# Performance work log

Measured on AMD Instinct MI355X. Metric: run time of the kernel, lower is better.

Reference implementation:

```python
import jax, jax.numpy as jnp
from jax import lax
import numpy as np


def conv2d(x, w, b=None, padding=0, dilation=1, groups=1):
    out = lax.conv_general_dilated(
        x, w, window_strides=(1, 1),
        padding=[(padding, padding), (padding, padding)],
        rhs_dilation=(dilation, dilation),
        dimension_numbers=('NCHW', 'OIHW', 'NCHW'),
        feature_group_count=groups)
    return out if b is None else out + b[None, :, None, None]


def hardswish(x):
    return x * jnp.clip(x + 3.0, 0.0, 6.0) / 6.0


def leaky(x, s):
    return jnp.where(x >= 0, x, s * x)


def bn_eval(x, g, b, eps=1e-5):
    # BatchNorm2d eval mode with running_mean=0, running_var=1
    scale = g * (1.0 / float(np.sqrt(1.0 + eps)))
    return x * scale[None, :, None, None] + b[None, :, None, None]


def deform_dw_conv(x, offset, w):
    # torchvision DeformConv2d, depthwise (groups=C), k=3, stride=1, pad=1, dil=1
    # x [B,C,H,W], offset [B,18,H,W] (y,x interleaved, kernel row-major), w [C,1,3,3]
    B, C, H, W = x.shape
    xf = x.reshape(B, C, H * W)
    yy = jnp.arange(H, dtype=x.dtype)[:, None]
    xx = jnp.arange(W, dtype=x.dtype)[None, :]
    out = jnp.zeros_like(x)
    for k in range(9):
        ky, kx = k // 3 - 1, k % 3 - 1
        py = yy + ky + offset[:, 2 * k]          # [B,H,W]
        px = xx + kx + offset[:, 2 * k + 1]
        y0 = jnp.floor(py)
        x0 = jnp.floor(px)
        wy = py - y0
        wx = px - x0
        y0i = y0.astype(jnp.int32)
        x0i = x0.astype(jnp.int32)
        val = jnp.zeros_like(x)
        for dy, dx, wgt in ((0, 0, (1 - wy) * (1 - wx)), (0, 1, (1 - wy) * wx),
                            (1, 0, wy * (1 - wx)), (1, 1, wy * wx)):
            iy = y0i + dy
            ix = x0i + dx
            valid = (iy >= 0) & (iy < H) & (ix >= 0) & (ix < W)
            idx = (jnp.clip(iy, 0, H - 1) * W + jnp.clip(ix, 0, W - 1)).reshape(B, 1, H * W)
            g = jnp.take_along_axis(xf, idx, axis=2).reshape(B, C, H, W)
            val = val + g * (wgt * valid.astype(x.dtype))[:, None]
        out = out + val * w[:, 0, ky + 1, kx + 1][None, :, None, None]
    return out


def patch_embed(x, off_dw, off_pw, dcn_w, pw_w):
    g = x.shape[1]
    off = conv2d(x, off_dw, padding=1, groups=g)
    off = jnp.clip(conv2d(off, off_pw), -1.0, 1.0)
    y = deform_dw_conv(x, off, dcn_w)
    return hardswish(conv2d(y, pw_w))


def depth_conv(x, dw_w, dw_b, pw_w, pw_b):
    g = x.shape[1]
    return conv2d(conv2d(x, dw_w, dw_b, padding=1, groups=g), pw_w, pw_b)


def cross_attn(hs, ctx, dw_w, dw_b, pw_w, pw_b):
    q = depth_conv(hs, dw_w[0], dw_b[0], pw_w[0], pw_b[0])
    k = depth_conv(ctx, dw_w[1], dw_b[1], pw_w[1], pw_b[1])
    v = depth_conv(ctx, dw_w[2], dw_b[2], pw_w[2], pw_b[2])
    head = q.shape[1] // 8  # num_heads = 8
    qt = q.transpose(0, 2, 1, 3)  # [B,H,C,W]
    kt = k.transpose(0, 2, 1, 3)
    vt = v.transpose(0, 2, 1, 3)
    scores = jnp.einsum('bhcw,bhdw->bhcd', qt, kt) / float(np.sqrt(head))
    probs = jax.nn.softmax(scores, axis=-1)
    o = jnp.einsum('bhcd,bhdw->bhcw', probs, vt)
    return o.transpose(0, 2, 1, 3)  # back to [B,C,H,W]


def dilated_block(x, ws, bs):
    h = x
    for i, d in enumerate((1, 2, 3, 2, 1)):
        h = conv2d(h, ws[i], bs[i], padding=d, dilation=d)
        if i < 4:
            h = leaky(h, 0.01)
    return h + x


def fft_block(h, fd1_w, fd2_w, fd1_g, fd1_bt, fd2_g, fd2_bt, fconv_w):
    Hh, Ww = h.shape[-2], h.shape[-1]
    xf = jnp.fft.rfft2(h)  # norm='backward'
    re, im = jnp.real(xf), jnp.imag(xf)
    mag = jnp.sqrt(re * re + im * im)
    pha = jnp.arctan2(im, re)

    def branch(m, i):
        t = leaky(bn_eval(conv2d(m, fd1_w[i]), fd1_g[i], fd1_bt[i]), 0.1)
        m1 = jnp.concatenate([m, t], 1)          # C+32
        t2 = leaky(bn_eval(conv2d(m1, fd2_w[i]), fd2_g[i], fd2_bt[i]), 0.1)
        m2 = jnp.concatenate([m1, t2], 1)        # C+64
        return conv2d(m2, fconv_w[i])            # back to C

    mag_o = branch(mag, 0)
    pha_o = branch(pha, 1)
    real = mag_o * jnp.cos(pha_o)
    imag = mag_o * jnp.sin(pha_o)
    out = jnp.fft.irfft2(lax.complex(real, imag), s=(Hh, Ww)) + h
    return out, mag_o, pha_o


def scarm_forward(x, ch_off_dw, ch_off_pw, ch_dcn_w, ch_pw,
                  ct_off_dw, ct_off_pw, ct_dcn_w, ct_pw,
                  db_w, db_b, ca_dw_w, ca_dw_b, ca_pw_w, ca_pw_b,
                  convHH_w, convHH_b, fd1_w, fd2_w, fd1_g, fd1_bt,
                  fd2_g, fd2_bt, fconv_w, conv_w, conv_b):
    b = x.shape[0]
    residual = x
    h = patch_embed(x, ch_off_dw, ch_off_pw, ch_dcn_w, ch_pw)  # [B,64,H,W]
    fft_out, mag, pha = fft_block(h, fd1_w, fd2_w, fd1_g, fd1_bt, fd2_g, fd2_bt, fconv_w)
    t = b // 3
    x_HL, x_LH, x_HH = h[:t], h[t:2 * t], h[2 * t:]
    # note: faithful to source, which aliases fft_LH/fft_HH back to x (h)
    fft_HL, fft_LH, fft_HH = fft_out[:t], h[t:2 * t], h[2 * t:]
    x_HH_LH = cross_attn(x_LH, x_HH, ca_dw_w[0], ca_dw_b[0], ca_pw_w[0], ca_pw_b[0])
    x_HH_HL = cross_attn(x_HL, x_HH, ca_dw_w[1], ca_dw_b[1], ca_pw_w[1], ca_pw_b[1])
    f_HH_LH = cross_attn(fft_LH, fft_HH, ca_dw_w[0], ca_dw_b[0], ca_pw_w[0], ca_pw_b[0])
    f_HH_HL = cross_attn(fft_HL, fft_HH, ca_dw_w[1], ca_dw_b[1], ca_pw_w[1], ca_pw_b[1])
    x_HL2 = dilated_block(x_HL, db_w[1], db_b[1])
    x_LH2 = dilated_block(x_LH, db_w[0], db_b[0])
    x_HH2 = dilated_block(conv2d(jnp.concatenate([x_HH_LH, x_HH_HL], 1), convHH_w, convHH_b, padding=1), db_w[2], db_b[2])
    f_HH2 = dilated_block(conv2d(jnp.concatenate([f_HH_LH, f_HH_HL], 1), convHH_w, convHH_b, padding=1), db_w[2], db_b[2])
    out = patch_embed(jnp.concatenate([x_HL2, x_LH2, x_HH2], 0), ct_off_dw, ct_off_pw, ct_dcn_w, ct_pw)
    fftout = patch_embed(jnp.concatenate([fft_HL, fft_LH, f_HH2], 0), ct_off_dw, ct_off_pw, ct_dcn_w, ct_pw)
    out = conv2d(jnp.concatenate([out, fftout], 1), conv_w, conv_b, padding=1)
    return out + residual, mag, pha


def setup_inputs() -> dict:
    key = jax.random.key(0)
    ks = iter(jax.random.split(key, 32))

    def rn(shape, scale):
        return jax.random.normal(next(ks), shape, jnp.float32) * scale

    return {
        'x': rn([12, 3, 128, 128], 1.0),
        'ch_off_dw': rn([3, 1, 3, 3], 0.3), 'ch_off_pw': rn([18, 3, 1, 1], 0.3),
        'ch_dcn_w': rn([3, 1, 3, 3], 0.3), 'ch_pw': rn([64, 3, 1, 1], 0.3),
        'ct_off_dw': rn([64, 1, 3, 3], 0.1), 'ct_off_pw': rn([18, 64, 1, 1], 0.1),
        'ct_dcn_w': rn([64, 1, 3, 3], 0.1), 'ct_pw': rn([3, 64, 1, 1], 0.05),
        'db_w': rn([3, 5, 64, 64, 3, 3], 0.05), 'db_b': rn([3, 5, 64], 0.01),
        'ca_dw_w': rn([2, 3, 64, 1, 3, 3], 0.3), 'ca_dw_b': rn([2, 3, 64], 0.01),
        'ca_pw_w': rn([2, 3, 64, 64, 1, 1], 0.1), 'ca_pw_b': rn([2, 3, 64], 0.01),
        'convHH_w': rn([64, 128, 3, 3], 0.03), 'convHH_b': rn([64], 0.01),
        'fd1_w': rn([2, 32, 64, 1, 1], 0.1), 'fd2_w': rn([2, 32, 96, 1, 1], 0.1),
        'fd1_g': 1.0 + rn([2, 32], 0.1), 'fd1_bt': rn([2, 32], 0.1),
        'fd2_g': 1.0 + rn([2, 32], 0.1), 'fd2_bt': rn([2, 32], 0.1),
        'fconv_w': rn([2, 64, 128, 1, 1], 0.1),
        'conv_w': rn([3, 6, 3, 3], 0.1), 'conv_b': rn([3], 0.01),
    }


def reference(x, ch_off_dw, ch_off_pw, ch_dcn_w, ch_pw,
              ct_off_dw, ct_off_pw, ct_dcn_w, ct_pw,
              db_w, db_b, ca_dw_w, ca_dw_b, ca_pw_w, ca_pw_b,
              convHH_w, convHH_b, fd1_w, fd2_w, fd1_g, fd1_bt,
              fd2_g, fd2_bt, fconv_w, conv_w, conv_b):
    return scarm_forward(x, ch_off_dw, ch_off_pw, ch_dcn_w, ch_pw,
                         ct_off_dw, ct_off_pw, ct_dcn_w, ct_pw,
                         db_w, db_b, ca_dw_w, ca_dw_b, ca_pw_w, ca_pw_b,
                         convHH_w, convHH_b, fd1_w, fd2_w, fd1_g, fd1_bt,
                         fd2_g, fd2_bt, fconv_w, conv_w, conv_b)
```

## Files before the change

### kernel.cpp

```cpp
#include <hip/hip_runtime.h>

namespace {

constexpr int Hn = 128, Wn = 128, HWn = 16384, HWFn = 8320;
constexpr float TWOPI = 6.2831853071795864769f;
constexpr float BN_SCALE = 0.99999500003749968f;

typedef __attribute__((ext_vector_type(8))) short short8;
typedef __attribute__((ext_vector_type(4))) float float4v;

__device__ __forceinline__ short f2bf(float v){
  unsigned u = __float_as_uint(v);
  u += 0x7FFF + ((u >> 16) & 1);
  return (short)(u >> 16);
}
__device__ __forceinline__ float bf2f(unsigned short u){
  return __uint_as_float(((unsigned)u) << 16);
}

__global__ void k_pack(const float* __restrict__ w, unsigned short* __restrict__ o,
                       int Cin, int csz, int n){
  int idx = blockIdx.x*256 + threadIdx.x;
  if (idx >= n) return;
  int ck = idx / csz;
  int i  = idx - ck*csz;
  const float* wp = w + (size_t)ck*csz;
  int j = i & 7, lane = (i>>3)&63, mt = (i>>9)&3, p = i>>11;
  int blk = p/18, r = p - blk*18, tap = r>>1, ks = r&1;
  int co = mt*16 + (lane & 15);
  int ci = blk*64 + ks*32 + ((lane>>4)<<3) + j;
  o[idx] = (unsigned short)f2bf(wp[((size_t)co*Cin + ci)*9 + tap]);
}

__global__ void k_packpw(const float* __restrict__ w, unsigned short* __restrict__ o,
                         int Cout, int MT, int n){
  int i = blockIdx.x*256 + threadIdx.x;
  if (i >= n) return;
  int per = MT << 10;
  int set = i / per;
  int r = i - set*per;
  int j = r & 7, lane = (r>>3)&63, blk = r>>9;
  int ks = blk / MT, mt = blk - ks*MT;
  int co = mt*16 + (lane & 15);
  int ci = ks*32 + ((lane>>4)<<3) + j;
  float v = (co < Cout) ? w[(size_t)set*Cout*64 + co*64 + ci] : 0.f;
  o[i] = (unsigned short)f2bf(v);
}

__global__ void k_wfdc(const float* __restrict__ fd1w, const float* __restrict__ fd2w,
                       const float* __restrict__ fcw,  const float* __restrict__ fd1g,
                       const float* __restrict__ fd2g, float* __restrict__ o){
  int i = blockIdx.x*256 + threadIdx.x;
  if (i >= 26624) return;
  int br = i / 13312, r = i - br*13312;
  float v;
  if (r < 2048){
    int ci = r >> 5, j = r & 31;
    v = fd1w[br*2048 + j*64 + ci] * (fd1g[br*32 + j]*BN_SCALE);
  } else if (r < 5120){
    int rr = r - 2048; int ci = rr >> 5, j = rr & 31;
    v = fd2w[br*3072 + j*96 + ci] * (fd2g[br*32 + j]*BN_SCALE);
  } else {
    int rr = r - 5120; int ci = rr >> 6, j = rr & 63;
    v = fcw[br*8192 + j*128 + ci];
  }
  o[i] = v;
}

__global__ __launch_bounds__(256) void k_fdc(
    const float* __restrict__ in, const float* __restrict__ wT,
    const float* __restrict__ bt1, const float* __restrict__ bt2,
    float* __restrict__ outp){
  __shared__ float tls[32*256];
  __shared__ float uls[32*256];
  int b = blockIdx.x, tile = blockIdx.y;
  int tid = threadIdx.x;
  int p = tile*256 + tid;
  bool act = p < HWFn;
  if (!act) p = HWFn - 1;
  const float* ip = in + (size_t)b*64*HWFn + p;
  float t[32];
  #pragma unroll
  for (int j=0;j<32;j++) t[j] = bt1[j];
  for (int ci=0; ci<64; ci++){
    float v = ip[(size_t)ci*HWFn];
    const float* w = wT + ci*32;
    #pragma unroll
    for (int j=0;j<32;j++) t[j] = fmaf(v, w[j], t[j]);
  }
  #pragma unroll
  for (int j=0;j<32;j++){
    float a = t[j]; tls[j*256+tid] = (a>=0.f)? a : 0.1f*a;
  }
  float u[32];
  #pragma unroll
  for (int j=0;j<32;j++) u[j] = bt2[j];
  for (int ci=0; ci<64; ci++){
    float v = ip[(size_t)ci*HWFn];
    const float* w = wT + 2048 + ci*32;
    #pragma unroll
    for (int j=0;j<32;j++) u[j] = fmaf(v, w[j], u[j]);
  }
  for (int ci=0; ci<32; ci++){
    float v = tls[ci*256+tid];
    const float* w = wT + 2048 + (64+ci)*32;
    #pragma unroll
    for (int j=0;j<32;j++) u[j] = fmaf(v, w[j], u[j]);
  }
  #pragma unroll
  for (int j=0;j<32;j++){
    float a = u[j]; uls[j*256+tid] = (a>=0.f)? a : 0.1f*a;
  }
  float acc[64];
  #pragma unroll
  for (int j=0;j<64;j++) acc[j] = 0.f;
  for (int ci=0; ci<64; ci++){
    float v = ip[(size_t)ci*HWFn];
    const float* w = wT + 5120 + ci*64;
    #pragma unroll
    for (int j=0;j<64;j++) acc[j] = fmaf(v, w[j], acc[j]);
  }
  for (int ci=0; ci<32; ci++){
    float v = tls[ci*256+tid];
    const float* w = wT + 5120 + (64+ci)*64;
    #pragma unroll
    for (int j=0;j<64;j++) acc[j] = fmaf(v, w[j], acc[j]);
  }
  for (int ci=0; ci<32; ci++){
    float v = uls[ci*256+tid];
    const float* w = wT + 5120 + (96+ci)*64;
    #pragma unroll
    for (int j=0;j<64;j++) acc[j] = fmaf(v, w[j], acc[j]);
  }
  if (act){
    float* op = outp + (size_t)b*64*HWFn + p;
    #pragma unroll
    for (int j=0;j<64;j++) op[(size_t)j*HWFn] = acc[j];
  }
}

constexpr int XST = 72;
__global__ __launch_bounds__(256) void k_mconv(
    const float* __restrict__ in, const float* __restrict__ in2,
    const unsigned short* __restrict__ wpk, const float* __restrict__ bias,
    const float* __restrict__ res, float* __restrict__ out,
    int nblk, int dl, int leaky){
  __shared__ short lds[3*134*XST];
  int b = blockIdx.x >> 7, y = blockIdx.x & 127;
  int tid = threadIdx.x;
  int wv = tid >> 6, lane = tid & 63;
  int nq = lane >> 4, nr = lane & 15;
  float4v acc[4][2];
  #pragma unroll
  for (int mt=0; mt<4; mt++)
    #pragma unroll
    for (int nt=0; nt<2; nt++) acc[mt][nt] = (float4v){0.f,0.f,0.f,0.f};

  for (int blk=0; blk<nblk; blk++){
    const float* src = blk ? in2 : in;
    __syncthreads();
    for (int e = tid; e < 3*64*32; e += 256){
      int dy = e >> 11;
      int r  = e & 2047;
      int ci = r >> 5;
      int xx = (r & 31) << 2;
      int yy = y + (dy-1)*dl;
      float4 v = make_float4(0.f,0.f,0.f,0.f);
      if (yy >= 0 && yy < Hn)
        v = *(const float4*)&src[(((size_t)b*64 + ci)*Hn + yy)*Wn + xx];
      short* d = &lds[(dy*134 + xx + 3)*XST + ci];
      d[0]     = f2bf(v.x);
      d[XST]   = f2bf(v.y);
      d[2*XST] = f2bf(v.z);
      d[3*XST] = f2bf(v.w);
    }
    for (int e = tid; e < 3*64*6; e += 256){
      int dy = e / 384; int r = e - dy*384;
      int ci = r / 6;   int k = r - ci*6;
      int x = (k < 3) ? k : 128 + k;
      lds[(dy*134 + x)*XST + ci] = 0;
    }
    __syncthreads();
    const unsigned short* wb = wpk + (size_t)blk*36864;
    for (int tap=0; tap<9; tap++){
      int dy = tap/3, dx = tap - (tap/3)*3;
      #pragma unroll
      for (int ks=0; ks<2; ks++){
        short8 a[4];
        #pragma unroll
        for (int mt=0; mt<4; mt++)
          a[mt] = *(const short8*)(wb + (((size_t)(tap*2+ks)*4+mt)<<9) + ((size_t)lane<<3));
        #pragma unroll
        for (int nt=0; nt<2; nt++){
          int x = wv*32 + nt*16 + nr + (dx-1)*dl + 3;
          short8 bf = *(const short8*)&lds[(dy*134 + x)*XST + ks*32 + nq*8];
          #pragma unroll
          for (int mt=0; mt<4; mt++)
            acc[mt][nt] = __builtin_amdgcn_mfma_f32_16x16x32_bf16(a[mt], bf, acc[mt][nt], 0, 0, 0);
        }
      }
    }
  }
  #pragma unroll
  for (int mt=0; mt<4; mt++)
  #pragma unroll
  for (int nt=0; nt<2; nt++){
    int x = wv*32 + nt*16 + nr;
    #pragma unroll
    for (int r2=0; r2<4; r2++){
      int co = mt*16 + nq*4 + r2;
      float a = acc[mt][nt][r2] + (bias ? bias[co] : 0.f);
      if (leaky) a = (a >= 0.f) ? a : 0.01f*a;
      size_t idx = (((size_t)b*64 + co)*Hn + y)*Wn + x;
      if (res) a += res[idx];
      out[idx] = a;
    }
  }
}

template<int MT>
__global__ __launch_bounds__(256) void k_dwpw(
    const float* __restrict__ in, const float* __restrict__ dww, const float* __restrict__ dwb,
    const unsigned short* __restrict__ pwpk, const float* __restrict__ pwb,
    float* __restrict__ out, int Cout, size_t outb, int post){
  __shared__ short tb[128*72];
  __shared__ float wsm[640];
  int b = blockIdx.x >> 7, y = blockIdx.x & 127;
  int tid = threadIdx.x;
  for (int i = tid; i < 640; i += 256)
    wsm[i] = (i < 576) ? dww[i] : (dwb ? dwb[i-576] : 0.f);
  __syncthreads();
  for (int e = tid; e < 2048; e += 256){
    int ci = e >> 5;
    int xx = (e & 31) << 2;
    const float* ip = in + ((size_t)b*64 + ci)*HWn;
    const float* wp = wsm + ci*9;
    float4 a0 = make_float4(0.f,0.f,0.f,0.f), a1 = a0, a2 = a0;
    float L0=0.f,L1=0.f,L2=0.f,R0=0.f,R1=0.f,R2=0.f;
    if (y > 0){
      const float* r = ip + (y-1)*Wn;
      a0 = *(const float4*)(r + xx);
      if (xx) L0 = r[xx-1];
      if (xx < 124) R0 = r[xx+4];
    }
    {
      const float* r = ip + y*Wn;
      a1 = *(const float4*)(r + xx);
      if (xx) L1 = r[xx-1];
      if (xx < 124) R1 = r[xx+4];
    }
    if (y < Hn-1){
      const float* r = ip + (y+1)*Wn;
      a2 = *(const float4*)(r + xx);
      if (xx) L2 = r[xx-1];
      if (xx < 124) R2 = r[xx+4];
    }
    float bb = wsm[576+ci];
    float o0=bb,o1=bb,o2=bb,o3=bb;
    float w0=wp[0],w1=wp[1],w2=wp[2];
    o0 = fmaf(w0,L0,  fmaf(w1,a0.x, fmaf(w2,a0.y, o0)));
    o1 = fmaf(w0,a0.x,fmaf(w1,a0.y, fmaf(w2,a0.z, o1)));
    o2 = fmaf(w0,a0.y,fmaf(w1,a0.z, fmaf(w2,a0.w, o2)));
    o3 = fmaf(w0,a0.z,fmaf(w1,a0.w, fmaf(w2,R0,   o3)));
    w0=wp[3];w1=wp[4];w2=wp[5];
    o0 = fmaf(w0,L1,  fmaf(w1,a1.x, fmaf(w2,a1.y, o0)));
    o1 = fmaf(w0,a1.x,fmaf(w1,a1.y, fmaf(w2,a1.z, o1)));
    o2 = fmaf(w0,a1.y,fmaf(w1,a1.z, fmaf(w2,a1.w, o2)));
    o3 = fmaf(w0,a1.z,fmaf(w1,a1.w, fmaf(w2,R1,   o3)));
    w0=wp[6];w1=wp[7];w2=wp[8];
    o0 = fmaf(w0,L2,  fmaf(w1,a2.x, fmaf(w2,a2.y, o0)));
    o1 = fmaf(w0,a2.x,fmaf(w1,a2.y, fmaf(w2,a2.z, o1)));
    o2 = fmaf(w0,a2.y,fmaf(w1,a2.z, fmaf(w2,a2.w, o2)));
    o3 = fmaf(w0,a2.z,fmaf(w1,a2.w, fmaf(w2,R2,   o3)));
    short* d = &tb[xx*72 + ci];
    d[0]   = f2bf(o0);
    d[72]  = f2bf(o1);
    d[144] = f2bf(o2);
    d[216] = f2bf(o3);
  }
  __syncthreads();
  int wv = tid>>6, lane = tid&63, nq = lane>>4, nr = lane&15;
  float4v acc[MT][2];
  #pragma unroll
  for (int mt=0; mt<MT; mt++)
    #pragma unroll
    for (int nt=0; nt<2; nt++) acc[mt][nt] = (float4v){0.f,0.f,0.f,0.f};
  #pragma unroll
  for (int ks=0; ks<2; ks++){
    short8 a[MT];
    #pragma unroll
    for (int mt=0; mt<MT; mt++)
      a[mt] = *(const short8*)(pwpk + ((ks*MT+mt)<<9) + (lane<<3));
    #pragma unroll
    for (int nt=0; nt<2; nt++){
      int x = wv*32 + nt*16 + nr;
      short8 bf = *(const short8*)&tb[x*72 + ks*32 + nq*8];
      #pragma unroll
      for (int mt=0; mt<MT; mt++)
        acc[mt][nt] = __builtin_amdgcn_mfma_f32_16x16x32_bf16(a[mt], bf, acc[mt][nt], 0, 0, 0);
    }
  }
  #pragma unroll
  for (int mt=0; mt<MT; mt++)
  #pragma unroll
  for (int nt=0; nt<2; nt++){
    int x = wv*32 + nt*16 + nr;
    #pragma unroll
    for (int r2=0; r2<4; r2++){
      int co = mt*16 + nq*4 + r2;
      if (co < Cout){
        float a = acc[mt][nt][r2] + (pwb ? pwb[co] : 0.f);
        if (post == 1) a = fminf(fmaxf(a, -1.f), 1.f);
        else if (post == 2) a = a*fminf(fmaxf(a+3.f, 0.f), 6.f)*(1.f/6.f);
        out[(size_t)b*outb + (size_t)co*HWn + y*Wn + x] = a;
      }
    }
  }
}

__global__ __launch_bounds__(512) void k_defpw(
    const float* __restrict__ xg, const float* __restrict__ off, const float* __restrict__ dcnw,
    const unsigned short* __restrict__ pwpk, float* __restrict__ out,
    int Cout, size_t outb, int post){
  __shared__ unsigned short xs[5*64*130];
  __shared__ short tb[128*72];
  __shared__ float wsm[576];
  int b = blockIdx.x >> 7, y = blockIdx.x & 127;
  int tid = threadIdx.x;
  int px = tid & 127, sub = tid >> 7;
  for (int i = tid; i < 576; i += 512) wsm[i] = dcnw[i];
  for (int e = tid; e < 10240; e += 512){
    int tr = e >> 11;
    int r  = e & 2047;
    int ci = r >> 5;
    int xx = (r & 31) << 2;
    int gy = min(max(y - 2 + tr, 0), Hn-1);
    float4 v = *(const float4*)&xg[(((size_t)b*64 + ci)*Hn + gy)*Wn + xx];
    unsigned short* d = &xs[(tr*64 + ci)*130 + xx];
    d[0] = (unsigned short)f2bf(v.x);
    d[1] = (unsigned short)f2bf(v.y);
    d[2] = (unsigned short)f2bf(v.z);
    d[3] = (unsigned short)f2bf(v.w);
  }
  const float* op = off + (size_t)b*18*HWn + y*Wn + px;
  int t0[9], t1[9], c0[9], c1[9];
  float w00[9], w01[9], w10[9], w11[9];
  #pragma unroll
  for (int k=0; k<9; k++){
    int ky = k/3 - 1, kx = k - (k/3)*3 - 1;
    float oy = op[(size_t)(2*k)*HWn];
    float ox = op[(size_t)(2*k+1)*HWn];
    float py = (float)(y + ky) + oy;
    float pxx = (float)(px + kx) + ox;
    float fy = floorf(py), fx = floorf(pxx);
    float wy = py - fy, wx = pxx - fx;
    int y0 = (int)fy, x0 = (int)fx;
    float vy0 = (y0 >= 0 && y0 < Hn) ? 1.f : 0.f;
    float vy1 = (y0+1 >= 0 && y0+1 < Hn) ? 1.f : 0.f;
    float vx0 = (x0 >= 0 && x0 < Wn) ? 1.f : 0.f;
    float vx1 = (x0+1 >= 0 && x0+1 < Wn) ? 1.f : 0.f;
    w00[k] = (1.f-wy)*(1.f-wx)*vy0*vx0;
    w01[k] = (1.f-wy)*wx*vy0*vx1;
    w10[k] = wy*(1.f-wx)*vy1*vx0;
    w11[k] = wy*wx*vy1*vx1;
    t0[k] = min(max(min(max(y0,   0), Hn-1) - (y-2), 0), 4);
    t1[k] = min(max(min(max(y0+1, 0), Hn-1) - (y-2), 0), 4);
    c0[k] = min(max(x0,   0), Wn-1);
    c1[k] = min(max(x0+1, 0), Wn-1);
  }
  __syncthreads();
  for (int ci = sub; ci < 64; ci += 4){
    float acc = 0.f;
    #pragma unroll
    for (int k=0; k<9; k++){
      const unsigned short* b0 = &xs[(t0[k]*64 + ci)*130];
      const unsigned short* b1 = &xs[(t1[k]*64 + ci)*130];
      float v = w00[k]*bf2f(b0[c0[k]]) + w01[k]*bf2f(b0[c1[k]])
              + w10[k]*bf2f(b1[c0[k]]) + w11[k]*bf2f(b1[c1[k]]);
      acc = fmaf(v, wsm[ci*9 + k], acc);
    }
    tb[px*72 + ci] = f2bf(acc);
  }
  __syncthreads();
  int wv = tid>>6, lane = tid&63, nq = lane>>4, nr = lane&15;
  float4v acc = (float4v){0.f,0.f,0.f,0.f};
  int x = wv*16 + nr;
  #pragma unroll
  for (int ks=0; ks<2; ks++){
    short8 a = *(const short8*)(pwpk + (ks<<9) + (lane<<3));
    short8 bf = *(const short8*)&tb[x*72 + ks*32 + nq*8];
    acc = __builtin_amdgcn_mfma_f32_16x16x32_bf16(a, bf, acc, 0, 0, 0);
  }
  #pragma unroll
  for (int r2=0; r2<4; r2++){
    int co = nq*4 + r2;
    if (co < Cout){
      float a = acc[r2];
      if (post == 2) a = a*fminf(fmaxf(a+3.f, 0.f), 6.f)*(1.f/6.f);
      out[(size_t)b*outb + (size_t)co*HWn + y*Wn + x] = a;
    }
  }
}

__global__ void k_dw3x3(const float* __restrict__ in, const float* __restrict__ w,
                        const float* __restrict__ bias, float* __restrict__ out, int C){
  int bc = blockIdx.x; int y = blockIdx.y; int x = threadIdx.x;
  int c = bc % C;
  const float* ip = in + (size_t)bc*HWn;
  const float* wp = w + c*9;
  float acc = bias ? bias[c] : 0.f;
  #pragma unroll
  for (int ky=0; ky<3; ky++){
    int yy = y + ky - 1; if (yy < 0 || yy >= Hn) continue;
    #pragma unroll
    for (int kx=0; kx<3; kx++){
      int xx = x + kx - 1; if (xx < 0 || xx >= Wn) continue;
      acc = fmaf(ip[yy*Wn+xx], wp[ky*3+kx], acc);
    }
  }
  out[(size_t)bc*HWn + y*Wn + x] = acc;
}

template<int CT>
__global__ void k_pwt(const float* __restrict__ in, const float* __restrict__ wg,
                      const float* __restrict__ bias, const float* __restrict__ bng,
                      const float* __restrict__ bnb, float* __restrict__ out,
                      int Cin, int Cout, int npix, int inb, int outb, int post, float slope){
  extern __shared__ float wsm[];
  int nt = (Cout + CT - 1)/CT;
  int b = blockIdx.x / nt, t = blockIdx.x - b*nt;
  int co0 = t*CT;
  for (int i = threadIdx.x; i < CT*Cin; i += 256){
    int co = i / Cin;
    wsm[i] = (co0 + co < Cout) ? wg[(size_t)(co0+co)*Cin + (i - co*Cin)] : 0.f;
  }
  __syncthreads();
  int p = blockIdx.y*256 + threadIdx.x;
  if (p >= npix) return;
  const float* ip = in + (size_t)b*inb + p;
  float acc[CT];
  #pragma unroll
  for (int j=0; j<CT; j++) acc[j] = 0.f;
  for (int ci=0; ci<Cin; ci++){
    float v = ip[(size_t)ci*npix];
    #pragma unroll
    for (int j=0; j<CT; j++) acc[j] = fmaf(v, wsm[j*Cin+ci], acc[j]);
  }
  #pragma unroll
  for (int j=0; j<CT; j++){
    int co = co0 + j;
    if (co < Cout){
      float a = acc[j] + (bias ? bias[co] : 0.f);
      if (bng) a = a*(bng[co]*BN_SCALE) + bnb[co];
      if (post == 1) a = fminf(fmaxf(a, -1.f), 1.f);
      else if (post == 2) a = a*fminf(fmaxf(a+3.f, 0.f), 6.f)*(1.f/6.f);
      else if (post == 3) a = (a >= 0.f) ? a : a*slope;
      out[(size_t)b*outb + (size_t)co*npix + p] = a;
    }
  }
}

__global__ void k_deform(const float* __restrict__ x, const float* __restrict__ off,
                         const float* __restrict__ w, float* __restrict__ out, int C){
  int bc = blockIdx.x; int b = bc / C; int c = bc - b*C;
  int y = blockIdx.y; int x0 = threadIdx.x;
  const float* xp = x + (size_t)bc*HWn;
  const float* op = off + (size_t)b*18*HWn + y*Wn + x0;
  const float* wp = w + c*9;
  float acc = 0.f;
  #pragma unroll
  for (int k=0; k<9; k++){
    int ky = k/3 - 1, kx = k - (k/3)*3 - 1;
    float oy = op[(size_t)(2*k)*HWn];
    float ox = op[(size_t)(2*k+1)*HWn];
    float py = (float)y + (float)ky + oy;
    float px = (float)x0 + (float)kx + ox;
    float fy = floorf(py), fx = floorf(px);
    float wy = py - fy, wx = px - fx;
    int y0 = (int)fy, xx0 = (int)fx;
    float val = 0.f;
    #pragma unroll
    for (int dy=0; dy<2; dy++){
      int iy = y0 + dy; if (iy < 0 || iy >= Hn) continue;
      float wyv = dy ? wy : (1.f - wy);
      #pragma unroll
      for (int dx=0; dx<2; dx++){
        int ix = xx0 + dx; if (ix < 0 || ix >= Wn) continue;
        float wxv = dx ? wx : (1.f - wx);
        val = fmaf(xp[iy*Wn+ix], wyv*wxv, val);
      }
    }
    acc = fmaf(val, wp[k], acc);
  }
  out[(size_t)bc*HWn + y*Wn + x0] = acc;
}

__global__ void k_conv3x3s(const float* __restrict__ in, const float* __restrict__ wgt,
                           const float* __restrict__ bias, const float* __restrict__ res,
                           float* __restrict__ out, int Cin, int Cout){
  int g = blockIdx.x;
  int b = g / Cout; int o0 = g - b*Cout;
  int y = blockIdx.y, x = threadIdx.x;
  float acc = bias ? bias[o0] : 0.f;
  for (int ci=0; ci<Cin; ci++){
    const float* iip = in + ((size_t)b*Cin + ci)*HWn;
    const float* wp = wgt + ((size_t)o0*Cin + ci)*9;
    #pragma unroll
    for (int ky=0; ky<3; ky++){
      int yy = y + ky - 1; if (yy < 0 || yy >= Hn) continue;
      #pragma unroll
      for (int kx=0; kx<3; kx++){
        int xx = x + kx - 1; if (xx < 0 || xx >= Wn) continue;
        acc = fmaf(iip[yy*Wn+xx], wp[ky*3+kx], acc);
      }
    }
  }
  size_t idx = ((size_t)b*Cout + o0)*HWn + y*Wn + x;
  if (res) acc += res[idx];
  out[idx] = acc;
}

__global__ __launch_bounds__(256) void k_attn(
    const float* __restrict__ q, const float* __restrict__ k,
    const float* __restrict__ v, float* __restrict__ o){
  __shared__ float qs[64][129];
  __shared__ float ks[64][129];
  __shared__ float vs[64][129];
  __shared__ float ps[64][66];
  int bh = blockIdx.x; int b = bh >> 7, h = bh & 127;
  size_t base = ((size_t)b*64*128 + h)*128;
  int tid = threadIdx.x;
  for (int e = tid; e < 8192; e += 256){
    int c = e >> 7, w = e & 127;
    size_t g = base + (size_t)c*HWn + w;
    qs[c][w] = q[g]; ks[c][w] = k[g]; vs[c][w] = v[g];
  }
  __syncthreads();
  {
    int c0 = (tid >> 4) << 2, d0 = (tid & 15) << 2;
    float acc[4][4];
    #pragma unroll
    for (int a=0; a<4; a++)
      #pragma unroll
      for (int bb=0; bb<4; bb++) acc[a][bb] = 0.f;
    for (int i=0; i<128; i++){
      float qv[4], kv[4];
      #pragma unroll
      for (int a=0; a<4; a++){ qv[a] = qs[c0+a][i]; kv[a] = ks[d0+a][i]; }
      #pragma unroll
      for (int a=0; a<4; a++)
        #pragma unroll
        for (int bb=0; bb<4; bb++) acc[a][bb] = fmaf(qv[a], kv[bb], acc[a][bb]);
    }
    #pragma unroll
    for (int a=0; a<4; a++)
      #pragma unroll
      for (int bb=0; bb<4; bb++)
        ps[c0+a][d0+bb] = acc[a][bb] * 0.35355339059327373f;
  }
  __syncthreads();
  {
    int wv = tid >> 6, lane = tid & 63;
    for (int it=0; it<16; it++){
      int row = wv*16 + it;
      float vv = ps[row][lane];
      float m = vv;
      #pragma unroll
      for (int off=32; off; off>>=1) m = fmaxf(m, __shfl_xor(m, off));
      float e = expf(vv - m);
      float s = e;
      #pragma unroll
      for (int off=32; off; off>>=1) s += __shfl_xor(s, off);
      ps[row][lane] = e / s;
    }
  }
  __syncthreads();
  {
    int c0 = (tid >> 4) << 2, w0 = (tid & 15) << 3;
    float acc[4][8];
    #pragma unroll
    for (int a=0; a<4; a++)
      #pragma unroll
      for (int j=0; j<8; j++) acc[a][j] = 0.f;
    for (int d=0; d<64; d++){
      float pv[4], vv[8];
      #pragma unroll
      for (int a=0; a<4; a++) pv[a] = ps[c0+a][d];
      #pragma unroll
      for (int j=0; j<8; j++) vv[j] = vs[d][w0+j];
      #pragma unroll
      for (int a=0; a<4; a++)
        #pragma unroll
        for (int j=0; j<8; j++) acc[a][j] = fmaf(pv[a], vv[j], acc[a][j]);
    }
    #pragma unroll
    for (int a=0; a<4; a++)
      #pragma unroll
      for (int j=0; j<8; j++)
        o[base + (size_t)(c0+a)*HWn + w0 + j] = acc[a][j];
  }
}

__device__ __forceinline__ float2 cmul(float2 a, float2 b){
  return make_float2(a.x*b.x - a.y*b.y, a.x*b.y + a.y*b.x);
}

__device__ __forceinline__ void wfft(float2& z0, float2& z1, const float2* twl, int l){
  {
    float dx = z0.x - z1.x, dy = z0.y - z1.y;
    z0.x += z1.x; z0.y += z1.y;
    z1 = cmul(make_float2(dx, dy), twl[6]);
  }
  #pragma unroll
  for (int s = 5; s >= 0; --s){
    int h = 1 << s;
    bool up = (l & h) != 0;
    float2 w = twl[s];
    {
      float ox = __shfl_xor(z0.x, h), oy = __shfl_xor(z0.y, h);
      float sx = up ? ox - z0.x : z0.x + ox;
      float sy = up ? oy - z0.y : z0.y + oy;
      float2 t = cmul(make_float2(sx, sy), w);
      z0.x = up ? t.x : sx;  z0.y = up ? t.y : sy;
    }
    {
      float ox = __shfl_xor(z1.x, h), oy = __shfl_xor(z1.y, h);
      float sx = up ? ox - z1.x : z1.x + ox;
      float sy = up ? oy - z1.y : z1.y + oy;
      float2 t = cmul(make_float2(sx, sy), w);
      z1.x = up ? t.x : sx;  z1.y = up ? t.y : sy;
    }
  }
}

__device__ __forceinline__ void wreorder(float2 z0, float2 z1, float2& n0, float2& n1, int l){
  int a = (int)(__brev((unsigned)(l >> 1)) >> 26);
  float p0x = __shfl(z0.x, a),   p0y = __shfl(z0.y, a);
  float p1x = __shfl(z1.x, a),   p1y = __shfl(z1.y, a);
  float q0x = __shfl(z0.x, a+1), q0y = __shfl(z0.y, a+1);
  float q1x = __shfl(z1.x, a+1), q1y = __shfl(z1.y, a+1);
  bool odd = (l & 1) != 0;
  n0 = odd ? make_float2(p1x, p1y) : make_float2(p0x, p0y);
  n1 = odd ? make_float2(q1x, q1y) : make_float2(q0x, q0y);
}

__global__ __launch_bounds__(256) void k_fft2(
    const float* __restrict__ x, float* __restrict__ mag, float* __restrict__ pha){
  __shared__ float2 sp[8320];
  int img = blockIdx.x;
  int tid = threadIdx.x;
  int wv = tid >> 6, l = tid & 63;
  float2 twl[7];
  #pragma unroll
  for (int s = 0; s < 7; ++s){
    int jh = (l & ((1 << s) - 1)) << (6 - s);
    float sv, cv; sincosf(-TWOPI * (float)jh * (1.f/128.f), &sv, &cv);
    twl[s] = make_float2(cv, sv);
  }
  const float* xp = x + (size_t)img*HWn;
  for (int f = wv; f < 64; f += 4){
    const float* r0 = xp + (2*f)*Wn;
    const float* r1 = xp + (2*f+1)*Wn;
    float2 z0 = make_float2(r0[l],      r1[l]);
    float2 z1 = make_float2(r0[64 + l], r1[64 + l]);
    wfft(z0, z1, twl, l);
    float2 n0, n1; wreorder(z0, z1, n0, n1, l);
    float zhx = __shfl(n1.x, (64 - l) & 63);
    float zhy = __shfl(n1.y, (64 - l) & 63);
    float2 Zn = (l == 0) ? n0 : make_float2(zhx, zhy);
    float2 A  = make_float2(0.5f*(n0.x + Zn.x), 0.5f*(n0.y - Zn.y));
    float2 Bv = make_float2(0.5f*(n0.y + Zn.y), 0.5f*(Zn.x - n0.x));
    sp[(2*f)*65 + l]   = A;
    sp[(2*f+1)*65 + l] = Bv;
    if (l == 0){
      sp[(2*f)*65 + 64]   = make_float2(n1.x, 0.f);
      sp[(2*f+1)*65 + 64] = make_float2(n1.y, 0.f);
    }
  }
  __syncthreads();
  for (int c = wv; c < 65; c += 4){
    float2 z0 = sp[l*65 + c];
    float2 z1 = sp[(64 + l)*65 + c];
    wfft(z0, z1, twl, l);
    float2 n0, n1; wreorder(z0, z1, n0, n1, l);
    sp[l*65 + c]        = make_float2(sqrtf(n0.x*n0.x + n0.y*n0.y), atan2f(n0.y, n0.x));
    sp[(64 + l)*65 + c] = make_float2(sqrtf(n1.x*n1.x + n1.y*n1.y), atan2f(n1.y, n1.x));
  }
  __syncthreads();
  float* mp = mag + (size_t)img*HWFn;
  float* pp = pha + (size_t)img*HWFn;
  for (int i = tid; i < 8320; i += 256){
    float2 v = sp[i];
    mp[i] = v.x; pp[i] = v.y;
  }
}

__global__ __launch_bounds__(256) void k_ifft2(
    const float* __restrict__ mo, const float* __restrict__ po,
    const float* __restrict__ hsrc, float* __restrict__ outp){
  __shared__ float2 sp[8320];
  int img = blockIdx.x;
  int tid = threadIdx.x;
  int wv = tid >> 6, l = tid & 63;
  float2 twl[7];
  #pragma unroll
  for (int s = 0; s < 7; ++s){
    int jh = (l & ((1 << s) - 1)) << (6 - s);
    float sv, cv; sincosf(TWOPI * (float)jh * (1.f/128.f), &sv, &cv);
    twl[s] = make_float2(cv, sv);
  }
  const float* mp = mo + (size_t)img*HWFn;
  const float* pp = po + (size_t)img*HWFn;
  for (int i = tid; i < 8320; i += 256){
    float m = mp[i], p = pp[i];
    float sv, cv; sincosf(p, &sv, &cv);
    sp[i] = make_float2(m*cv, m*sv);
  }
  __syncthreads();
  for (int c = wv; c < 65; c += 4){
    float2 z0 = sp[l*65 + c];
    float2 z1 = sp[(64 + l)*65 + c];
    wfft(z0, z1, twl, l);
    float2 n0, n1; wreorder(z0, z1, n0, n1, l);
    sp[l*65 + c]        = n0;
    sp[(64 + l)*65 + c] = n1;
  }
  __syncthreads();
  const float scl = 1.f/16384.f;
  for (int f = wv; f < 64; f += 4){
    float2 A  = sp[(2*f)*65 + l];
    float2 Bv = sp[(2*f+1)*65 + l];
    if (l == 0){ A.y = 0.f; Bv.y = 0.f; }
    float2 z0 = make_float2(A.x - Bv.y, A.y + Bv.x);
    int lm = 64 - l;
    float2 Am = sp[(2*f)*65 + lm];
    float2 Bm = sp[(2*f+1)*65 + lm];
    float2 z1 = (l == 0) ? make_float2(Am.x, Bm.x)
                         : make_float2(Am.x + Bm.y, Bm.x - Am.y);
    wfft(z0, z1, twl, l);
    float2 n0, n1; wreorder(z0, z1, n0, n1, l);
    size_t g0 = (size_t)img*HWn + (size_t)(2*f)*Wn + l;
    size_t g1 = g0 + Wn;
    outp[g0]      = n0.x*scl + hsrc[g0];
    outp[g0 + 64] = n1.x*scl + hsrc[g0 + 64];
    outp[g1]      = n0.y*scl + hsrc[g1];
    outp[g1 + 64] = n1.y*scl + hsrc[g1 + 64];
  }
}

}

extern "C" void kernel_launch(void* const* d_in, const int* in_sizes, int n_in,
                              void* d_out, int out_size, void* d_ws, size_t ws_size,
                              hipStream_t stream){
  const float *xf   =(const float*)d_in[0],  *chodw=(const float*)d_in[1],
              *chopw=(const float*)d_in[2],  *chdcn=(const float*)d_in[3],
              *chpw =(const float*)d_in[4],  *ctodw=(const float*)d_in[5],
              *ctopw=(const float*)d_in[6],  *ctdcn=(const float*)d_in[7],
              *ctpw =(const float*)d_in[8],  *dbw  =(const float*)d_in[9],
              *dbb  =(const float*)d_in[10], *cadw =(const float*)d_in[11],
              *cadb =(const float*)d_in[12], *capw =(const float*)d_in[13],
              *capb =(const float*)d_in[14], *hhw  =(const float*)d_in[15],
              *hhb  =(const float*)d_in[16], *fd1w =(const float*)d_in[17],
              *fd2w =(const float*)d_in[18], *fd1g =(const float*)d_in[19],
              *fd1bt=(const float*)d_in[20], *fd2g =(const float*)d_in[21],
              *fd2bt=(const float*)d_in[22], *fcw  =(const float*)d_in[23],
              *cw   =(const float*)d_in[24], *cb   =(const float*)d_in[25];

  constexpr size_t M = 1048576;
  float* ws = (float*)d_ws;
  float* h     = ws;
  float* fftHL = ws + 12*M;
  float* cat6  = ws + 16*M;
  unsigned short* wpkDB = (unsigned short*)(cat6 + 1179648);
  unsigned short* wpkHH = wpkDB + 552960;
  float* wfdc = (float*)(wpkHH + 73728);
  float* P = cat6 + 1179648 + 313344 + 26624;

  const int NB = (ws_size >= 266018816ull) ? 4 : 1;
  const size_t S = (size_t)NB*M;
  float* kb  = P;        float* vb  = P + S;   float* qb  = P + 2*S;
  float* qsl = P + 3*S;
  float* aA  = P + 4*S;  float* aB  = P + 5*S;
  float* aC  = P + 6*S;  float* hh1 = P + 7*S; float* sA  = P + 8*S;
  float* sB  = P + 9*S;  float* dbuf= P + 10*S;
  float* X   = P + 11*S;
  unsigned short* pwpkCA = (unsigned short*)qsl;
  unsigned short* pwpkTO = pwpkCA + 24576;
  unsigned short* pwpkTP = pwpkTO + 2048;
  float* dwb3 = P; float* offb12 = P + 589824; float* yb3 = P + 4128768;

  float* out = (float*)d_out;
  float* out0 = out;
  float* out1 = out + 589824;
  float* out2 = out + 589824 + 6389760;

  auto PW = [&](const float* in, const float* wg, const float* bi, const float* g, const float* bt,
                float* o, int B, int Ci, int Co, int npix, int inb, int outb, int post, float slope){
    int py = (npix + 255)/256;
    if (Co > 32){
      k_pwt<32><<<dim3(B*2, py), 256, 32*Ci*4, stream>>>(in, wg, bi, g, bt, o, Ci, Co, npix, inb, outb, post, slope);
    } else if (Co > 18){
      k_pwt<32><<<dim3(B, py), 256, 32*Ci*4, stream>>>(in, wg, bi, g, bt, o, Ci, Co, npix, inb, outb, post, slope);
    } else if (Co > 3){
      k_pwt<18><<<dim3(B, py), 256, 18*Ci*4, stream>>>(in, wg, bi, g, bt, o, Ci, Co, npix, inb, outb, post, slope);
    } else {
      k_pwt<3><<<dim3(B, py), 256, 3*Ci*4, stream>>>(in, wg, bi, g, bt, o, Ci, Co, npix, inb, outb, post, slope);
    }
  };
  auto MCONV = [&](const float* in, const float* in2, const unsigned short* wp, const float* bi,
                   const float* res, float* o, int B, int nblk, int dl, int lk){
    k_mconv<<<B*128, 256, 0, stream>>>(in, in2, wp, bi, res, o, nblk, dl, lk);
  };
  auto DILm = [&](const float* in, int set, const float* bset, int B){
    const unsigned short* w5 = wpkDB + (size_t)set*5*36864;
    MCONV(in, nullptr, w5,          bset,      nullptr, sA,   B, 1, 1, 1);
    MCONV(sA, nullptr, w5+36864,    bset+64,   nullptr, sB,   B, 1, 2, 1);
    MCONV(sB, nullptr, w5+2*36864,  bset+128,  nullptr, sA,   B, 1, 3, 1);
    MCONV(sA, nullptr, w5+3*36864,  bset+192,  nullptr, sB,   B, 1, 2, 1);
    MCONV(sB, nullptr, w5+4*36864,  bset+256,  in,      dbuf, B, 1, 1, 0);
  };
  auto DCONVm = [&](const float* in, int idx, float* o, int B){
    k_dwpw<4><<<B*128, 256, 0, stream>>>(in, cadw + idx*576, cadb + idx*64,
        pwpkCA + (size_t)idx*4096, capb + idx*64, o, 64, (size_t)64*HWn, 0);
  };
  auto ATTNm = [&](const float* qsrc, int qidx, float* o, int B){
    DCONVm(qsrc, qidx, qb, B);
    k_attn<<<B*128, 256, 0, stream>>>(qb, kb, vb, o);
  };
  auto PEMBEDm = [&](const float* in, float* outSlice, int B){
    k_dwpw<2><<<B*128, 256, 0, stream>>>(in, ctodw, nullptr, pwpkTO, nullptr,
        X, 18, (size_t)18*HWn, 1);
    k_defpw<<<B*128, 512, 0, stream>>>(in, X, ctdcn, pwpkTP, outSlice, 3, (size_t)6*HWn, 2);
  };

  k_pack<<<(552960 + 255)/256, 256, 0, stream>>>(dbw, wpkDB, 64, 36864, 552960);
  k_pack<<<288, 256, 0, stream>>>(hhw, wpkHH, 128, 73728, 73728);
  k_wfdc<<<104, 256, 0, stream>>>(fd1w, fd2w, fcw, fd1g, fd2g, wfdc);

  k_dw3x3<<<dim3(36, Hn), 128, 0, stream>>>(xf, chodw, nullptr, dwb3, 3);
  PW(dwb3, chopw, nullptr, nullptr, nullptr, offb12, 12, 3, 18, HWn, 3*HWn, 18*HWn, 1, 0.f);
  k_deform<<<dim3(36, Hn), 128, 0, stream>>>(xf, offb12, chdcn, yb3, 3);
  PW(yb3, chpw, nullptr, nullptr, nullptr, h, 12, 3, 64, HWn, 3*HWn, 64*HWn, 2, 0.f);

  if (NB == 4){
    float* mB = P;
    float* pB = P + 6389760;
    k_fft2<<<768, 256, 0, stream>>>(h, mB, pB);
    k_fdc<<<dim3(12, 33), 256, 0, stream>>>(mB, wfdc,         fd1bt,      fd2bt,      out1);
    k_fdc<<<dim3(12, 33), 256, 0, stream>>>(pB, wfdc + 13312, fd1bt + 32, fd2bt + 32, out2);
    k_ifft2<<<256, 256, 0, stream>>>(out1, out2, h, fftHL);
  } else {
    float* mB = P;
    float* pB = P + 2129920;
    for (int c=0; c<3; c++){
      const float* hsrc = h + (size_t)c*4*M;
      float* o1 = out1 + (size_t)c*2129920;
      float* o2 = out2 + (size_t)c*2129920;
      k_fft2<<<256, 256, 0, stream>>>(hsrc, mB, pB);
      k_fdc<<<dim3(4, 33), 256, 0, stream>>>(mB, wfdc,         fd1bt,      fd2bt,      o1);
      k_fdc<<<dim3(4, 33), 256, 0, stream>>>(pB, wfdc + 13312, fd1bt + 32, fd2bt + 32, o2);
      if (c == 0)
        k_ifft2<<<256, 256, 0, stream>>>(out1, out2, h, fftHL);
    }
  }

  k_packpw<<<96, 256, 0, stream>>>(capw,  pwpkCA, 64, 4, 24576);
  k_packpw<<<8,  256, 0, stream>>>(ctopw, pwpkTO, 18, 2, 2048);
  k_packpw<<<4,  256, 0, stream>>>(ctpw,  pwpkTP, 3,  1, 1024);

  for (int g0=0; g0<4; g0+=NB){
    const float* hHL = h + (size_t)g0*M;
    const float* hLH = h + (size_t)(4+g0)*M;
    const float* hHH = h + (size_t)(8+g0)*M;
    const float* fHL = fftHL + (size_t)g0*M;
    DCONVm(hHH, 1, kb, NB);
    DCONVm(hHH, 2, vb, NB);
    ATTNm(hLH, 0, aA, NB);
    DCONVm(hHH, 4, kb, NB);
    DCONVm(hHH, 5, vb, NB);
    ATTNm(hHL, 3, aB, NB);
    ATTNm(fHL, 3, aC, NB);
    MCONV(aA, aB, wpkHH, hhb, nullptr, hh1, NB, 2, 1, 0);
    DILm(hh1, 2, dbb + 2*320, NB);
    PEMBEDm(dbuf, cat6 + (size_t)((8+g0)*6)*HWn, NB);
    MCONV(aA, aC, wpkHH, hhb, nullptr, hh1, NB, 2, 1, 0);
    DILm(hh1, 2, dbb + 2*320, NB);
    PEMBEDm(dbuf, cat6 + (size_t)((8+g0)*6+3)*HWn, NB);
    DILm(hHL, 1, dbb + 320, NB);
    PEMBEDm(dbuf, cat6 + (size_t)(g0*6)*HWn, NB);
    DILm(hLH, 0, dbb, NB);
    PEMBEDm(dbuf, cat6 + (size_t)((4+g0)*6)*HWn, NB);
    PEMBEDm(fHL, cat6 + (size_t)(g0*6+3)*HWn, NB);
    PEMBEDm(hLH, cat6 + (size_t)((4+g0)*6+3)*HWn, NB);
  }

  k_conv3x3s<<<dim3(36, Hn), 128, 0, stream>>>(cat6, cw, cb, xf, out0, 6, 3);
}
```

Measured before the change: 1.733 ms.

## Split k_fdc output channels across warps with 64-pixel tiles and LDS sharing

Restructures the frequency-domain conv kernel so each block handles 64 pixels, with its four wavefronts each computing a slice of the output channels (8, 8, then 16). Intermediate activations are shared through LDS with barriers between stages. The grid grows from 33 to 130 tiles per batch. This cuts per-thread register pressure and raises parallelism and occupancy. The cost is four redundant reads of the input per pixel and extra synchronization.

```diff
diff --git a/kernel.cpp b/kernel.cpp
--- a/kernel.cpp
+++ b/kernel.cpp
@@ -71,72 +71,78 @@
     const float* __restrict__ in, const float* __restrict__ wT,
     const float* __restrict__ bt1, const float* __restrict__ bt2,
     float* __restrict__ outp){
-  __shared__ float tls[32*256];
-  __shared__ float uls[32*256];
+  __shared__ float tls[32][64];
+  __shared__ float uls[32][64];
   int b = blockIdx.x, tile = blockIdx.y;
   int tid = threadIdx.x;
-  int p = tile*256 + tid;
-  bool act = p < HWFn;
-  if (!act) p = HWFn - 1;
-  const float* ip = in + (size_t)b*64*HWFn + p;
-  float t[32];
-  #pragma unroll
-  for (int j=0;j<32;j++) t[j] = bt1[j];
+  int lane = tid & 63;
+  int kk = __builtin_amdgcn_readfirstlane(tid >> 6);
+  const float* ip = in + (size_t)b*64*HWFn + tile*64 + lane;
+  {
+    float t[8];
+    #pragma unroll
+    for (int jj=0;jj<8;jj++) t[jj] = bt1[kk*8+jj];
+    for (int ci=0; ci<64; ci++){
+      float v = ip[(size_t)ci*HWFn];
+      const float* w = wT + ci*32 + kk*8;
+      #pragma unroll
+      for (int jj=0;jj<8;jj++) t[jj] = fmaf(v, w[jj], t[jj]);
+    }
+    #pragma unroll
+    for (int jj=0;jj<8;jj++){
+      float a = t[jj];
+      tls[kk*8+jj][lane] = (a>=0.f)? a : 0.1f*a;
+    }
+  }
+  __syncthreads();
+  {
+    float u[8];
+    #pragma unroll
+    for (int jj=0;jj<8;jj++) u[jj] = bt2[kk*8+jj];
+    for (int ci=0; ci<64; ci++){
+      float v = ip[(size_t)ci*HWFn];
+      const float* w = wT + 2048 + ci*32 + kk*8;
+      #pragma unroll
+      for (int jj=0;jj<8;jj++) u[jj] = fmaf(v, w[jj], u[jj]);
+    }
+    for (int ci=0; ci<32; ci++){
+      float v = tls[ci][lane];
+      const float* w = wT + 2048 + (64+ci)*32 + kk*8;
+      #pragma unroll
+      for (int jj=0;jj<8;jj++) u[jj] = fmaf(v, w[jj], u[jj]);
+    }
+    #pragma unroll
+    for (int jj=0;jj<8;jj++){
+      float a = u[jj];
+      uls[kk*8+jj][lane] = (a>=0.f)? a : 0.1f*a;
+    }
+  }
+  __syncthreads();
+  float acc[16];
+  #pragma unroll
+  for (int jj=0;jj<16;jj++) acc[jj] = 0.f;
   for (int ci=0; ci<64; ci++){
     float v = ip[(size_t)ci*HWFn];
-    const float* w = wT + ci*32;
-    #pragma unroll
-    for (int j=0;j<32;j++) t[j] = fmaf(v, w[j], t[j]);
-  }
-  #pragma unroll
-  for (int j=0;j<32;j++){
-    float a = t[j]; tls[j*256+tid] = (a>=0.f)? a : 0.1f*a;
-  }
-  float u[32];
-  #pragma unroll
-  for (int j=0;j<32;j++) u[j] = bt2[j];
-  for (int ci=0; ci<64; ci++){
-    float v = ip[(size_t)ci*HWFn];
-    const float* w = wT + 2048 + ci*32;
-    #pragma unroll
-    for (int j=0;j<32;j++) u[j] = fmaf(v, w[j], u[j]);
+    const float* w = wT + 5120 + ci*64 + kk*16;
+    #pragma unroll
+    for (int jj=0;jj<16;jj++) acc[jj] = fmaf(v, w[jj], acc[jj]);
   }
   for (int ci=0; ci<32; ci++){
-    float v = tls[ci*256+tid];
-    const float* w = wT + 2048 + (64+ci)*32;
-    #pragma unroll
-    for (int j=0;j<32;j++) u[j] = fmaf(v, w[j], u[j]);
-  }
-  #pragma unroll
-  for (int j=0;j<32;j++){
-    float a = u[j]; uls[j*256+tid] = (a>=0.f)? a : 0.1f*a;
-  }
-  float acc[64];
-  #pragma unroll
-  for (int j=0;j<64;j++) acc[j] = 0.f;
-  for (int ci=0; ci<64; ci++){
-    float v = ip[(size_t)ci*HWFn];
-    const float* w = wT + 5120 + ci*64;
-    #pragma unroll
-    for (int j=0;j<64;j++) acc[j] = fmaf(v, w[j], acc[j]);
+    float v = tls[ci][lane];
+    const float* w = wT + 5120 + (64+ci)*64 + kk*16;
+    #pragma unroll
+    for (int jj=0;jj<16;jj++) acc[jj] = fmaf(v, w[jj], acc[jj]);
   }
   for (int ci=0; ci<32; ci++){
-    float v = tls[ci*256+tid];
-    const float* w = wT + 5120 + (64+ci)*64;
-    #pragma unroll
-    for (int j=0;j<64;j++) acc[j] = fmaf(v, w[j], acc[j]);
-  }
-  for (int ci=0; ci<32; ci++){
-    float v = uls[ci*256+tid];
-    const float* w = wT + 5120 + (96+ci)*64;
-    #pragma unroll
-    for (int j=0;j<64;j++) acc[j] = fmaf(v, w[j], acc[j]);
-  }
-  if (act){
-    float* op = outp + (size_t)b*64*HWFn + p;
-    #pragma unroll
-    for (int j=0;j<64;j++) op[(size_t)j*HWFn] = acc[j];
-  }
+    float v = uls[ci][lane];
+    const float* w = wT + 5120 + (96+ci)*64 + kk*16;
+    #pragma unroll
+    for (int jj=0;jj<16;jj++) acc[jj] = fmaf(v, w[jj], acc[jj]);
+  }
+  float* op = outp + (size_t)b*64*HWFn + tile*64 + lane;
+  #pragma unroll
+  for (int jj=0;jj<16;jj++)
+    op[(size_t)(kk*16+jj)*HWFn] = acc[jj];
 }
 
 constexpr int XST = 72;
@@ -847,8 +853,8 @@
     float* mB = P;
     float* pB = P + 6389760;
     k_fft2<<<768, 256, 0, stream>>>(h, mB, pB);
-    k_fdc<<<dim3(12, 33), 256, 0, stream>>>(mB, wfdc,         fd1bt,      fd2bt,      out1);
-    k_fdc<<<dim3(12, 33), 256, 0, stream>>>(pB, wfdc + 13312, fd1bt + 32, fd2bt + 32, out2);
+    k_fdc<<<dim3(12, 130), 256, 0, stream>>>(mB, wfdc,         fd1bt,      fd2bt,      out1);
+    k_fdc<<<dim3(12, 130), 256, 0, stream>>>(pB, wfdc + 13312, fd1bt + 32, fd2bt + 32, out2);
     k_ifft2<<<256, 256, 0, stream>>>(out1, out2, h, fftHL);
   } else {
     float* mB = P;
@@ -858,8 +864,8 @@
       float* o1 = out1 + (size_t)c*2129920;
       float* o2 = out2 + (size_t)c*2129920;
       k_fft2<<<256, 256, 0, stream>>>(hsrc, mB, pB);
-      k_fdc<<<dim3(4, 33), 256, 0, stream>>>(mB, wfdc,         fd1bt,      fd2bt,      o1);
-      k_fdc<<<dim3(4, 33), 256, 0, stream>>>(pB, wfdc + 13312, fd1bt + 32, fd2bt + 32, o2);
+      k_fdc<<<dim3(4, 130), 256, 0, stream>>>(mB, wfdc,         fd1bt,      fd2bt,      o1);
+      k_fdc<<<dim3(4, 130), 256, 0, stream>>>(pB, wfdc + 13312, fd1bt + 32, fd2bt + 32, o2);
       if (c == 0)
         k_ifft2<<<256, 256, 0, stream>>>(out1, out2, h, fftHL);
     }
```

Result: no change. 1.761 ms (+1.6%).
